# Kernel optimization log

Hardware: AMD Instinct MI355X
Metric: run time of the kernel (lower is better)

The kernel has to match this reference:

```python
import jax, jax.numpy as jnp
import numpy as np

N = 8192          # codeword length (power of 2)
K = 4096          # info bits (rate 1/2)
BS = 8192         # batch of codewords


def _gen_indices(n):
    """Stage-wise gather indices for the Arikan butterfly.
    Row s: position ind_dest XORs with ind_dest + 2**s; all other positions
    gather the sentinel column n, which holds a constant 0 (XOR identity)."""
    nb_stages = int(np.log2(n))
    ind = np.full((nb_stages, n + 1), n, dtype=np.int32)
    for s in range(nb_stages):
        r = np.arange(n // 2)
        ind_dest = r * 2 - (r % (2 ** s))
        ind[s, ind_dest] = ind_dest + 2 ** s
    return ind


def setup_inputs() -> dict:
    key = jax.random.key(0)
    u = jax.random.randint(key, (BS, K), 0, 2).astype(jnp.float32)  # info bits in {0,1}
    frozen_pos = np.arange(N - K)
    info_pos = jnp.asarray(np.setdiff1d(np.arange(N), frozen_pos), dtype=jnp.int32)
    ind_gather = jnp.asarray(_gen_indices(N))  # [log2(N), N+1] int32
    return {"u": u, "info_pos": info_pos, "ind_gather": ind_gather}


def reference(u, info_pos, ind_gather):
    bs = u.shape[0]
    n = ind_gather.shape[1] - 1
    nb_stages = ind_gather.shape[0]
    # scatter info bits into codeword positions (frozen positions stay 0)
    c = jnp.zeros((bs, n), dtype=u.dtype).at[:, info_pos].set(u)
    # append the zero sentinel column used as XOR identity
    x = jnp.concatenate([c, jnp.zeros((bs, 1), dtype=u.dtype)], axis=1)  # [bs, n+1]
    for s in range(nb_stages):  # fixed log2(n) structurally-distinct stages
        x = (x + x[:, ind_gather[s]]) % 2  # XOR on {0,1} bits
    return x[:, :n]
```

## Files before the change

### kernel.cpp

```cpp
#include <hip/hip_runtime.h>


constexpr int ROWS      = 8192;
constexpr int K_WORDS   = 1024;
constexpr int OUT_WORDS = 2048;

__global__ __launch_bounds__(256)
void polar_encode_kernel(const uint4* __restrict__ u, uint4* __restrict__ out) {
    const int lane = threadIdx.x & 63;
    const int row  = (blockIdx.x << 2) + (threadIdx.x >> 6);

    const uint4* urow = u + (size_t)row * K_WORDS;

    uint4 v[16];
#pragma unroll
    for (int r = 0; r < 16; ++r) v[r] = urow[(r << 6) + lane];

#pragma unroll
    for (int r = 0; r < 16; ++r) { v[r].x ^= v[r].y; v[r].z ^= v[r].w; }
#pragma unroll
    for (int r = 0; r < 16; ++r) { v[r].x ^= v[r].z; v[r].y ^= v[r].w; }

#pragma unroll
    for (int s = 0; s < 6; ++s) {
        const unsigned m = ((lane >> s) & 1) ? 0u : 0xFFFFFFFFu;
#pragma unroll
        for (int r = 0; r < 16; ++r) {
            unsigned px = (unsigned)__shfl_xor((int)v[r].x, 1 << s, 64);
            unsigned py = (unsigned)__shfl_xor((int)v[r].y, 1 << s, 64);
            unsigned pz = (unsigned)__shfl_xor((int)v[r].z, 1 << s, 64);
            unsigned pw = (unsigned)__shfl_xor((int)v[r].w, 1 << s, 64);
            v[r].x ^= px & m;
            v[r].y ^= py & m;
            v[r].z ^= pz & m;
            v[r].w ^= pw & m;
        }
    }

#pragma unroll
    for (int s = 0; s < 4; ++s) {
#pragma unroll
        for (int r = 0; r < 16; ++r) {
            if (!(r & (1 << s))) {
                const int p = r | (1 << s);
                v[r].x ^= v[p].x;
                v[r].y ^= v[p].y;
                v[r].z ^= v[p].z;
                v[r].w ^= v[p].w;
            }
        }
    }

    uint4* orow = out + (size_t)row * OUT_WORDS;
#pragma unroll
    for (int r = 0; r < 16; ++r) {
        const int o = (r << 6) + lane;
        orow[o]           = v[r];
        orow[K_WORDS + o] = v[r];
    }
}

extern "C" void kernel_launch(void* const* d_in, const int* in_sizes, int n_in,
                              void* d_out, int out_size, void* d_ws, size_t ws_size,
                              hipStream_t stream) {
    (void)in_sizes; (void)n_in; (void)d_ws; (void)ws_size; (void)out_size;
    const uint4* u = (const uint4*)d_in[0];
    uint4* out = (uint4*)d_out;

    dim3 grid(ROWS / 4);
    dim3 block(256);
    hipLaunchKernelGGL(polar_encode_kernel, grid, block, 0, stream, u, out);
}
```

Before: 363.6 us.

## Split each row across a block with LDS exchange and a double-buffered persistent loop

Each row is now handled by a whole 256-thread block instead of one wavefront. The last two butterfly stages, which cross wavefronts, are finished by exchanging partial results through shared memory between barriers. Blocks are persistent (2048 of them) and double-buffer the load of the next row while the current one is processed and stored. Loads and stores use nontemporal hints. This cuts register pressure and raises memory-level parallelism for a bandwidth-bound kernel, at the cost of two barriers and LDS traffic per row.

```diff
diff --git a/kernel.cpp b/kernel.cpp
--- a/kernel.cpp
+++ b/kernel.cpp
@@ -1,31 +1,32 @@
 #include <hip/hip_runtime.h>
 
+
+typedef unsigned int u32x4 __attribute__((ext_vector_type(4)));
 
 constexpr int ROWS      = 8192;
 constexpr int K_WORDS   = 1024;
 constexpr int OUT_WORDS = 2048;
+constexpr int NBLOCKS   = 2048;
 
-__global__ __launch_bounds__(256)
-void polar_encode_kernel(const uint4* __restrict__ u, uint4* __restrict__ out) {
-    const int lane = threadIdx.x & 63;
-    const int row  = (blockIdx.x << 2) + (threadIdx.x >> 6);
+__device__ __forceinline__ void load_row4(u32x4 (&v)[4],
+                                          const u32x4* __restrict__ urow,
+                                          int t) {
+#pragma unroll
+    for (int r = 0; r < 4; ++r)
+        v[r] = __builtin_nontemporal_load(&urow[(r << 8) + t]);
+}
 
-    const uint4* urow = u + (size_t)row * K_WORDS;
-
-    uint4 v[16];
+__device__ __forceinline__ void inreg_stages(u32x4 (&v)[4], int lane) {
 #pragma unroll
-    for (int r = 0; r < 16; ++r) v[r] = urow[(r << 6) + lane];
-
+    for (int r = 0; r < 4; ++r) { v[r].x ^= v[r].y; v[r].z ^= v[r].w; }
 #pragma unroll
-    for (int r = 0; r < 16; ++r) { v[r].x ^= v[r].y; v[r].z ^= v[r].w; }
-#pragma unroll
-    for (int r = 0; r < 16; ++r) { v[r].x ^= v[r].z; v[r].y ^= v[r].w; }
+    for (int r = 0; r < 4; ++r) { v[r].x ^= v[r].z; v[r].y ^= v[r].w; }
 
 #pragma unroll
     for (int s = 0; s < 6; ++s) {
         const unsigned m = ((lane >> s) & 1) ? 0u : 0xFFFFFFFFu;
 #pragma unroll
-        for (int r = 0; r < 16; ++r) {
+        for (int r = 0; r < 4; ++r) {
             unsigned px = (unsigned)__shfl_xor((int)v[r].x, 1 << s, 64);
             unsigned py = (unsigned)__shfl_xor((int)v[r].y, 1 << s, 64);
             unsigned pz = (unsigned)__shfl_xor((int)v[r].z, 1 << s, 64);
@@ -37,26 +38,65 @@
         }
     }
 
+    v[0] ^= v[1]; v[2] ^= v[3];
+    v[0] ^= v[2]; v[1] ^= v[3];
+}
+
+__device__ __forceinline__ void process_store(u32x4 (&v)[4],
+                                              u32x4* __restrict__ orow,
+                                              u32x4 (*__restrict__ xch)[64],
+                                              int lane, int wv, int t) {
+    inreg_stages(v, lane);
+
+    asm volatile("s_barrier" ::: "memory");
 #pragma unroll
-    for (int s = 0; s < 4; ++s) {
+    for (int r = 0; r < 4; ++r) xch[(r << 2) + wv][lane] = v[r];
+    asm volatile("s_waitcnt lgkmcnt(0)\n\ts_barrier" ::: "memory");
+
+    if (wv == 0) {
 #pragma unroll
-        for (int r = 0; r < 16; ++r) {
-            if (!(r & (1 << s))) {
-                const int p = r | (1 << s);
-                v[r].x ^= v[p].x;
-                v[r].y ^= v[p].y;
-                v[r].z ^= v[p].z;
-                v[r].w ^= v[p].w;
-            }
-        }
+        for (int r = 0; r < 4; ++r)
+            v[r] ^= xch[(r << 2) + 1][lane] ^ xch[(r << 2) + 2][lane]
+                                            ^ xch[(r << 2) + 3][lane];
+    } else if (wv != 3) {
+#pragma unroll
+        for (int r = 0; r < 4; ++r)
+            v[r] ^= xch[(r << 2) + 3][lane];
     }
 
-    uint4* orow = out + (size_t)row * OUT_WORDS;
 #pragma unroll
-    for (int r = 0; r < 16; ++r) {
-        const int o = (r << 6) + lane;
-        orow[o]           = v[r];
-        orow[K_WORDS + o] = v[r];
+    for (int r = 0; r < 4; ++r) {
+        const int w = (r << 8) + t;
+        __builtin_nontemporal_store(v[r], &orow[w]);
+        __builtin_nontemporal_store(v[r], &orow[K_WORDS + w]);
+    }
+}
+
+__global__ __launch_bounds__(256, 4)
+void polar_encode_kernel(const u32x4* __restrict__ u, u32x4* __restrict__ out) {
+    __shared__ u32x4 xch[16][64];
+
+    const int t    = threadIdx.x;
+    const int lane = t & 63;
+    const int wv   = t >> 6;
+
+    int row = blockIdx.x;
+    u32x4 A[4], B[4];
+
+    load_row4(A, u + (size_t)row * K_WORDS, t);
+
+    while (true) {
+        int n = row + NBLOCKS;
+        if (n < ROWS) load_row4(B, u + (size_t)n * K_WORDS, t);
+        process_store(A, out + (size_t)row * OUT_WORDS, xch, lane, wv, t);
+        if (n >= ROWS) break;
+        row = n;
+
+        n = row + NBLOCKS;
+        if (n < ROWS) load_row4(A, u + (size_t)n * K_WORDS, t);
+        process_store(B, out + (size_t)row * OUT_WORDS, xch, lane, wv, t);
+        if (n >= ROWS) break;
+        row = n;
     }
 }
 
@@ -64,10 +104,10 @@
                               void* d_out, int out_size, void* d_ws, size_t ws_size,
                               hipStream_t stream) {
     (void)in_sizes; (void)n_in; (void)d_ws; (void)ws_size; (void)out_size;
-    const uint4* u = (const uint4*)d_in[0];
-    uint4* out = (uint4*)d_out;
+    const u32x4* u = (const u32x4*)d_in[0];
+    u32x4* out = (u32x4*)d_out;
 
-    dim3 grid(ROWS / 4);
+    dim3 grid(NBLOCKS);
     dim3 block(256);
     hipLaunchKernelGGL(polar_encode_kernel, grid, block, 0, stream, u, out);
 }
```

Result: no change. 357.3 us (-1.7%).
